# Performance work log

Measured on AMD Instinct MI355X. Metric: run time of the kernel, lower is better.

## Reference

```python
import jax, jax.numpy as jnp
import numpy as np

NEG = -1000000000.0

def setup_inputs() -> dict:
    key = jax.random.key(0)
    ks = jax.random.split(key, 6)
    B, V, F, H = 8, 4, 256, 768
    video_features = jax.random.normal(ks[0], (B, V, F, H), dtype=jnp.float32)
    video_attention_mask = jax.random.randint(ks[1], (B, V, F), 0, 2) > 0  # True = masked
    s = 1.0 / np.sqrt(H)
    Wqkv = jax.random.normal(ks[2], (3 * H, H), dtype=jnp.float32) * s
    bqkv = jax.random.normal(ks[3], (3 * H,), dtype=jnp.float32) * 0.01
    Wo = jax.random.normal(ks[4], (H, H), dtype=jnp.float32) * s
    bo = jax.random.normal(ks[5], (H,), dtype=jnp.float32) * 0.01
    return {"video_features": video_features, "video_attention_mask": video_attention_mask,
            "Wqkv": Wqkv, "bqkv": bqkv, "Wo": Wo, "bo": bo}

def reference(video_features, video_attention_mask, Wqkv, bqkv, Wo, bo):
    B, V, F, H = video_features.shape
    n_heads = 12
    head_dim = H // n_heads
    S = V * F  # total frames
    x = video_features.reshape(B, S, H)
    mask = video_attention_mask.reshape(B, S)
    # fused QKV projection (torch Linear: x @ W.T + b)
    qkv = x @ Wqkv.T + bqkv                      # [B, S, 3H]
    qkv = qkv.reshape(B, S, n_heads, 3 * head_dim).transpose(0, 2, 1, 3)  # [B, h, S, 3d]
    q, k, v = jnp.split(qkv, 3, axis=-1)         # each [B, h, S, d]
    scores = jnp.einsum('bhqd,bhkd->bhqk', q, k) / np.sqrt(head_dim)
    scores = jnp.where(mask[:, None, None, :], NEG, scores)
    attn = jax.nn.softmax(scores, axis=-1)       # dropout p=0 (eval) -> identity
    out = jnp.einsum('bhqk,bhkd->bhqd', attn, v) # [B, h, S, d]
    out = out.transpose(0, 2, 1, 3).reshape(B, S, H)
    out = out @ Wo.T + bo
    return out.reshape(B, V, F, H)
```

## Files before the change

### kernel.cpp

```cpp
#include <hip/hip_runtime.h>
#include <stdint.h>

typedef unsigned short u16;
typedef unsigned int u32;
typedef __attribute__((ext_vector_type(8))) unsigned short u16x8;
typedef __attribute__((ext_vector_type(4))) unsigned short u16x4;
typedef __attribute__((ext_vector_type(2))) unsigned int u32x2;
typedef __attribute__((ext_vector_type(4))) float f32x4;
typedef __attribute__((ext_vector_type(16))) float f32x16;
typedef __attribute__((ext_vector_type(4))) float floatx4;
typedef __attribute__((ext_vector_type(8))) __bf16 bf16x8;


__device__ __forceinline__ u16 f2bf(float f) {
  union { float f; unsigned u; } c; c.f = f;
  unsigned r = c.u + 0x7fffu + ((c.u >> 16) & 1u);
  return (u16)(r >> 16);
}

__device__ __forceinline__ u32 packbf2(float lo, float hi) {
  return (u32)f2bf(lo) | ((u32)f2bf(hi) << 16);
}

__device__ __forceinline__ u32 cvtpk(float lo, float hi) {
  u32 r;
  asm("v_cvt_pk_bf16_f32 %0, %1, %2" : "=v"(r) : "v"(lo), "v"(hi));
  return r;
}

__device__ __forceinline__ bf16x8 ld_bf8(const u16* p) {
  return __builtin_bit_cast(bf16x8, *(const u16x8*)p);
}

__device__ __forceinline__ float fexp2(float x) {
#if __has_builtin(__builtin_amdgcn_exp2f)
  return __builtin_amdgcn_exp2f(x);
#else
  float r; asm("v_exp_f32 %0, %1" : "=v"(r) : "v"(x)); return r;
#endif
}

__device__ __forceinline__ void glds16(const void* g, void* l) {
  __builtin_amdgcn_global_load_lds(
      (const __attribute__((address_space(1))) void*)g,
      (__attribute__((address_space(3))) void*)l, 16, 0, 0);
}

__global__ void convert_kernel(const float* __restrict__ x,
                               const float* __restrict__ w1,
                               const float* __restrict__ w2,
                               u16* __restrict__ xb,
                               u16* __restrict__ w1b,
                               u16* __restrict__ w2b) {
  const long NX = 6291456 / 4, NW1 = 1769472 / 4, NW2 = 589824 / 4;
  const long total = NX + NW1 + NW2;
  for (long i = (long)blockIdx.x * 256 + threadIdx.x; i < total;
       i += (long)gridDim.x * 256) {
    const float* src; u16* dst; long j;
    if (i < NX)            { src = x;  dst = xb;  j = i; }
    else if (i < NX + NW1) { src = w1; dst = w1b; j = i - NX; }
    else                   { src = w2; dst = w2b; j = i - NX - NW1; }
    floatx4 v = ((const floatx4*)src)[j];
    u16x4 o;
    o[0] = f2bf(v[0]); o[1] = f2bf(v[1]); o[2] = f2bf(v[2]); o[3] = f2bf(v[3]);
    ((u16x4*)dst)[j] = o;
  }
}

__global__ __launch_bounds__(256, 2)
void qkv_gemm(const u16* __restrict__ A, const u16* __restrict__ W,
              const float* __restrict__ bias,
              u16* __restrict__ qb, u16* __restrict__ kb, u16* __restrict__ vtb) {
  __shared__ __align__(16) u16 lds[30720];
  const int tid = threadIdx.x;
  const int lane = tid & 63, wid = tid >> 6;
  const int wm = wid >> 1, wn = wid & 1;
  const int l15 = lane & 15, l4 = lane >> 4;

  const int p = blockIdx.x;
  const int xcd = p & 7, i = p >> 3;
  const int by = xcd * 8 + i / 12;
  const int bx = i % 12;
  const int rowA0 = by * 128, rowB0 = bx * 192;

  const int rlo = lane >> 3;
  const u16* gA[2];
  const u16* gB[3];
#pragma unroll
  for (int c = 0; c < 2; ++c) {
    int mr = wid * 16 + c * 8 + rlo;
    int sl = (lane & 7) ^ (mr & 7);
    gA[c] = A + (size_t)(rowA0 + 2 * mr + (sl >> 2)) * 768 + (sl & 3) * 8;
  }
#pragma unroll
  for (int c = 0; c < 3; ++c) {
    int mr = wid * 24 + c * 8 + rlo;
    int sl = (lane & 7) ^ (mr & 7);
    gB[c] = W + (size_t)(rowB0 + 2 * mr + (sl >> 2)) * 768 + (sl & 3) * 8;
  }

  f32x4 acc[4][6];
  const f32x4 vz = {0.f, 0.f, 0.f, 0.f};
#pragma unroll
  for (int mi = 0; mi < 4; ++mi)
#pragma unroll
    for (int nj = 0; nj < 6; ++nj) acc[mi][nj] = vz;

#define QSTAGE(kb_, k0_)                                                   \
  {                                                                        \
    u16* bA_ = lds + (kb_) * 4096;                                         \
    u16* bB_ = lds + 12288 + (kb_) * 6144;                                 \
    _Pragma("unroll") for (int c = 0; c < 2; ++c)                          \
        glds16(gA[c] + (k0_), bA_ + (wid * 16 + c * 8) * 64);              \
    _Pragma("unroll") for (int c = 0; c < 3; ++c)                          \
        glds16(gB[c] + (k0_), bB_ + (wid * 24 + c * 8) * 64);              \
  }

  QSTAGE(0, 0);
  QSTAGE(1, 32);

  for (int ks = 0; ks < 24; ++ks) {
    const int cb = ks % 3;
    const u16* cA = lds + cb * 4096;
    const u16* cB = lds + 12288 + cb * 6144;

    __builtin_amdgcn_s_barrier();
    if (ks < 22) {
      QSTAGE((ks + 2) % 3, (ks + 2) * 32);
      asm volatile("s_waitcnt vmcnt(10)" ::: "memory");
    } else if (ks == 22) {
      asm volatile("s_waitcnt vmcnt(5)" ::: "memory");
    } else {
      asm volatile("s_waitcnt vmcnt(0)" ::: "memory");
    }
    __builtin_amdgcn_s_barrier();
    __builtin_amdgcn_sched_barrier(0);

    bf16x8 af[4], bfr[6];
#pragma unroll
    for (int mi = 0; mi < 4; ++mi) {
      int m = wm * 64 + mi * 16 + l15;
      int mr = m >> 1;
      int sp = ((m & 1) * 4 + l4) ^ (mr & 7);
      af[mi] = ld_bf8(cA + mr * 64 + sp * 8);
    }
#pragma unroll
    for (int nj = 0; nj < 6; ++nj) {
      int n = wn * 96 + nj * 16 + l15;
      int mr = n >> 1;
      int sp = ((n & 1) * 4 + l4) ^ (mr & 7);
      bfr[nj] = ld_bf8(cB + mr * 64 + sp * 8);
    }
    __builtin_amdgcn_s_setprio(1);
#pragma unroll
    for (int mi = 0; mi < 4; ++mi)
#pragma unroll
      for (int nj = 0; nj < 6; ++nj)
        acc[mi][nj] = __builtin_amdgcn_mfma_f32_16x16x32_bf16(
            af[mi], bfr[nj], acc[mi][nj], 0, 0, 0);
    __builtin_amdgcn_s_setprio(0);
  }
#undef QSTAGE

  const float QSC = 0.125f * 1.44269504088896f;
  const int batch = by >> 3, s0 = (by & 7) * 128;
  const size_t gbase = (size_t)(batch * 12 + bx) * 65536;

  float bias_v[6];
#pragma unroll
  for (int nj = 0; nj < 6; ++nj)
    bias_v[nj] = bias[rowB0 + wn * 96 + nj * 16 + l15];

  __syncthreads();

#pragma unroll
  for (int nj = 0; nj < 6; ++nj) {
    int col0 = wn * 96 + nj * 16;
    int band = col0 >> 6;
    int dd = (col0 & 63) + l15;
    float bv = bias_v[nj];
    if (band < 2) {
      float sc = (band == 0) ? QSC : 1.0f;
      u16* reg = lds + band * 9216;
#pragma unroll
      for (int mi = 0; mi < 4; ++mi)
#pragma unroll
        for (int r = 0; r < 4; ++r) {
          int m = wm * 64 + mi * 16 + l4 * 4 + r;
          reg[m * 72 + dd] = f2bf((acc[mi][nj][r] + bv) * sc);
        }
    } else {
      u16* reg = lds + 18432;
#pragma unroll
      for (int mi = 0; mi < 4; ++mi)
#pragma unroll
        for (int r = 0; r < 4; r += 2) {
          int m = wm * 64 + mi * 16 + l4 * 4 + r;
          *(u32*)&reg[dd * 136 + m] =
              packbf2(acc[mi][nj][r] + bv, acc[mi][nj][r + 1] + bv);
        }
    }
  }
  __syncthreads();

#pragma unroll
  for (int j = 0; j < 4; ++j) {
    int c = tid + j * 256;
    int m = c >> 3, dd0 = (c & 7) << 3;
    u16x8 v = *(const u16x8*)&lds[m * 72 + dd0];
    *(u16x8*)&qb[gbase + (size_t)(s0 + m) * 64 + dd0] = v;
  }
#pragma unroll
  for (int j = 0; j < 4; ++j) {
    int c = tid + j * 256;
    int m = c >> 3, dd0 = (c & 7) << 3;
    u16x8 v = *(const u16x8*)&lds[9216 + m * 72 + dd0];
    *(u16x8*)&kb[gbase + (size_t)(s0 + m) * 64 + dd0] = v;
  }
#pragma unroll
  for (int j = 0; j < 4; ++j) {
    int c = tid + j * 256;
    int dd = c >> 4, m0 = (c & 15) << 3;
    u16x8 v = *(const u16x8*)&lds[18432 + dd * 136 + m0];
    *(u16x8*)&vtb[gbase + (size_t)dd * 1024 + s0 + m0] = v;
  }
}

__global__ __launch_bounds__(256, 3)
void attn_kernel(const u16* __restrict__ qb, const u16* __restrict__ kb,
                 const u16* __restrict__ vtb, const void* __restrict__ maskp,
                 u16* __restrict__ x2) {
  const int bh = blockIdx.x, qt = blockIdx.y;
  const int b = bh / 12, h = bh - b * 12;
  const int tid = threadIdx.x;
  const int w = tid >> 6, lane = tid & 63;
  const int l31 = lane & 31, hi = lane >> 5;

  __shared__ float mbias[1024];
  __shared__ int any_big;
  __shared__ __align__(16) u16 plds[4][32][40];
  __shared__ __align__(16) u16 kvs[16384];

  if (tid == 0) any_big = 0;
  __syncthreads();
  {
    const unsigned* mu = (const unsigned*)maskp;
    int loc = 0;
    for (int i = tid; i < 2048; i += 256)
      if (mu[i] > 1u) loc = 1;
    if (loc) atomicOr(&any_big, 1);
  }
  __syncthreads();
  const float CEXP = 23.0831206542234f;
  if (any_big) {
    const unsigned char* mb = (const unsigned char*)maskp;
    for (int i = tid; i < 1024; i += 256)
      mbias[i] = mb[b * 1024 + i] ? -100000.0f : -CEXP;
  } else {
    const int* mi_ = (const int*)maskp;
    for (int i = tid; i < 1024; i += 256)
      mbias[i] = mi_[b * 1024 + i] ? -100000.0f : -CEXP;
  }

  const size_t base = (size_t)bh * 65536;
  const int q0w = qt * 128 + w * 32;

  const int rlo = lane >> 3;
  const int cg = (lane & 7) ^ (rlo & 7);
  const int srow = w * 8 + rlo;
  const u16* kg0 = kb + base + (size_t)srow * 64 + cg * 8;
  const u16* vg0 = vtb + base + (size_t)srow * 1024 + cg * 8;
  u16* kd0 = kvs + w * 512;
  u16* vd0 = kvs + 4096 + w * 512;

  bf16x8 qf[4];
#pragma unroll
  for (int dstep = 0; dstep < 4; ++dstep)
    qf[dstep] = ld_bf8(qb + base + (size_t)(q0w + l31) * 64 + dstep * 16 + hi * 8);

  f32x16 o[2];
#pragma unroll
  for (int dh = 0; dh < 2; ++dh)
#pragma unroll
    for (int r = 0; r < 16; ++r) o[dh][r] = 0.f;
  float ps = 0.f;

  glds16(kg0, kd0);
  glds16(kg0 + 32 * 64, kd0 + 2048);
  glds16(vg0, vd0);
  glds16(vg0 + 32 * 1024, vd0 + 2048);
  __syncthreads();

  for (int kt = 0; kt < 16; ++kt) {
    const int cur = kt & 1;
    if (kt < 15) {
      const int nxt = cur ^ 1;
      glds16(kg0 + (kt + 1) * 4096, kd0 + nxt * 8192);
      glds16(kg0 + (kt + 1) * 4096 + 32 * 64, kd0 + nxt * 8192 + 2048);
      glds16(vg0 + (kt + 1) * 64, vd0 + nxt * 8192);
      glds16(vg0 + (kt + 1) * 64 + 32 * 1024, vd0 + nxt * 8192 + 2048);
    }

    const u16* Kl = kvs + cur * 8192;
    const u16* Vl = kvs + cur * 8192 + 4096;

#pragma unroll
    for (int kk = 0; kk < 2; ++kk) {
      f32x16 s;
#pragma unroll
      for (int r = 0; r < 16; ++r) s[r] = 0.f;
      const int rk = kk * 32 + l31;
      __builtin_amdgcn_s_setprio(1);
#pragma unroll
      for (int dstep = 0; dstep < 4; ++dstep) {
        bf16x8 kf = ld_bf8(Kl + rk * 64 + ((dstep * 2 + hi) ^ (rk & 7)) * 8);
        s = __builtin_amdgcn_mfma_f32_32x32x16_bf16(kf, qf[dstep], s, 0, 0, 0);
      }
      __builtin_amdgcn_s_setprio(0);
#pragma unroll
      for (int g = 0; g < 4; ++g) {
        f32x4 bv = *(const f32x4*)(mbias + kt * 64 + kk * 32 + g * 8 + hi * 4);
        float p0 = fexp2(s[g * 4 + 0] + bv[0]);
        float p1 = fexp2(s[g * 4 + 1] + bv[1]);
        float p2 = fexp2(s[g * 4 + 2] + bv[2]);
        float p3 = fexp2(s[g * 4 + 3] + bv[3]);
        ps += (p0 + p1) + (p2 + p3);
        const int colb = g * 8 + hi * 4;
        *(u32*)&plds[w][l31][colb]     = cvtpk(p0, p1);
        *(u32*)&plds[w][l31][colb + 2] = cvtpk(p2, p3);
      }

      __builtin_amdgcn_s_setprio(1);
#pragma unroll
      for (int t = 0; t < 2; ++t) {
        bf16x8 pf = ld_bf8(&plds[w][l31][t * 16 + hi * 8]);
#pragma unroll
        for (int dh = 0; dh < 2; ++dh) {
          const int rv = dh * 32 + l31;
          const int gv = kk * 4 + t * 2 + hi;
          bf16x8 vf = ld_bf8(Vl + rv * 64 + (gv ^ (rv & 7)) * 8);
          o[dh] = __builtin_amdgcn_mfma_f32_32x32x16_bf16(vf, pf, o[dh], 0, 0, 0);
        }
      }
      __builtin_amdgcn_s_setprio(0);
    }

    __syncthreads();
  }

  ps += __shfl_xor(ps, 32, 64);
  float inv = 1.0f / ps;

  u16* obuf = kvs + w * 2304;
#pragma unroll
  for (int dh = 0; dh < 2; ++dh)
#pragma unroll
    for (int j = 0; j < 8; ++j) {
      u32 v = cvtpk(o[dh][2 * j] * inv, o[dh][2 * j + 1] * inv);
      int col = dh * 32 + 8 * (j >> 1) + 4 * hi + 2 * (j & 1);
      *(u32*)(obuf + l31 * 72 + col) = v;
    }

  {
    int row2 = lane >> 1, ch = lane & 1;
    const u16* srcp = obuf + row2 * 72 + ch * 32;
    u16x8 t0 = *(const u16x8*)(srcp);
    u16x8 t1 = *(const u16x8*)(srcp + 8);
    u16x8 t2 = *(const u16x8*)(srcp + 16);
    u16x8 t3 = *(const u16x8*)(srcp + 24);
    size_t m = (size_t)b * 1024 + qt * 128 + w * 32 + row2;
    u16* dst = x2 + m * 768 + h * 64 + ch * 32;
    *(u16x8*)dst = t0;
    *(u16x8*)(dst + 8) = t1;
    *(u16x8*)(dst + 16) = t2;
    *(u16x8*)(dst + 24) = t3;
  }
}

__global__ __launch_bounds__(256, 2)
void out_gemm(const u16* __restrict__ A, const u16* __restrict__ W,
              const float* __restrict__ bias, float* __restrict__ out) {
  __shared__ __align__(16) u16 lds[24576];
  const int tid = threadIdx.x;
  const int lane = tid & 63, wid = tid >> 6;
  const int wm = wid >> 1, wn = wid & 1;
  const int l15 = lane & 15, l4 = lane >> 4;

  const int p = blockIdx.x;
  const int xcd = p & 7, i = p >> 3;
  const int by = xcd * 16 + (i >> 2);
  const int bx = i & 3;
  const int rowA0 = by * 64, rowB0 = bx * 192;

  const int rlo = lane >> 3;
  const u16* gA0;
  {
    int mr = wid * 8 + rlo;
    int sl = (lane & 7) ^ (mr & 7);
    gA0 = A + (size_t)(rowA0 + 2 * mr + (sl >> 2)) * 768 + (sl & 3) * 8;
  }
  const u16* gB[3];
#pragma unroll
  for (int c = 0; c < 3; ++c) {
    int mr = wid * 24 + c * 8 + rlo;
    int sl = (lane & 7) ^ (mr & 7);
    gB[c] = W + (size_t)(rowB0 + 2 * mr + (sl >> 2)) * 768 + (sl & 3) * 8;
  }

  f32x4 acc[2][6];
  const f32x4 vz = {0.f, 0.f, 0.f, 0.f};
#pragma unroll
  for (int mi = 0; mi < 2; ++mi)
#pragma unroll
    for (int nj = 0; nj < 6; ++nj) acc[mi][nj] = vz;

#define OSTAGE(kb_, k0_)                                                   \
  {                                                                        \
    u16* bA_ = lds + (kb_) * 2048;                                         \
    u16* bB_ = lds + 6144 + (kb_) * 6144;                                  \
    glds16(gA0 + (k0_), bA_ + (wid * 8) * 64);                             \
    _Pragma("unroll") for (int c = 0; c < 3; ++c)                          \
        glds16(gB[c] + (k0_), bB_ + (wid * 24 + c * 8) * 64);              \
  }

  OSTAGE(0, 0);
  OSTAGE(1, 32);

  for (int ks = 0; ks < 24; ++ks) {
    const int cb = ks % 3;
    const u16* cA = lds + cb * 2048;
    const u16* cB = lds + 6144 + cb * 6144;

    __builtin_amdgcn_s_barrier();
    if (ks < 22) {
      OSTAGE((ks + 2) % 3, (ks + 2) * 32);
      asm volatile("s_waitcnt vmcnt(8)" ::: "memory");
    } else if (ks == 22) {
      asm volatile("s_waitcnt vmcnt(4)" ::: "memory");
    } else {
      asm volatile("s_waitcnt vmcnt(0)" ::: "memory");
    }
    __builtin_amdgcn_s_barrier();
    __builtin_amdgcn_sched_barrier(0);

    bf16x8 af[2], bfr[6];
#pragma unroll
    for (int mi = 0; mi < 2; ++mi) {
      int m = wm * 32 + mi * 16 + l15;
      int mr = m >> 1;
      int sp = ((m & 1) * 4 + l4) ^ (mr & 7);
      af[mi] = ld_bf8(cA + mr * 64 + sp * 8);
    }
#pragma unroll
    for (int nj = 0; nj < 6; ++nj) {
      int n = wn * 96 + nj * 16 + l15;
      int mr = n >> 1;
      int sp = ((n & 1) * 4 + l4) ^ (mr & 7);
      bfr[nj] = ld_bf8(cB + mr * 64 + sp * 8);
    }
    __builtin_amdgcn_s_setprio(1);
#pragma unroll
    for (int mi = 0; mi < 2; ++mi)
#pragma unroll
      for (int nj = 0; nj < 6; ++nj)
        acc[mi][nj] = __builtin_amdgcn_mfma_f32_16x16x32_bf16(
            af[mi], bfr[nj], acc[mi][nj], 0, 0, 0);
    __builtin_amdgcn_s_setprio(0);
  }
#undef OSTAGE

#pragma unroll
  for (int nj = 0; nj < 6; ++nj) {
    int n = rowB0 + wn * 96 + nj * 16 + l15;
    float bn_ = bias[n];
#pragma unroll
    for (int mi = 0; mi < 2; ++mi)
#pragma unroll
      for (int r = 0; r < 4; ++r) {
        int m = rowA0 + wm * 32 + mi * 16 + l4 * 4 + r;
        out[(size_t)m * 768 + n] = acc[mi][nj][r] + bn_;
      }
  }
}

extern "C" void kernel_launch(void* const* d_in, const int* in_sizes, int n_in,
                              void* d_out, int out_size, void* d_ws, size_t ws_size,
                              hipStream_t stream) {
  const float* x    = (const float*)d_in[0];
  const void*  mask = d_in[1];
  const float* wqkv = (const float*)d_in[2];
  const float* bqkv = (const float*)d_in[3];
  const float* wo   = (const float*)d_in[4];
  const float* bo   = (const float*)d_in[5];
  float* out = (float*)d_out;

  u16* ws = (u16*)d_ws;
  u16* xbf   = ws;
  u16* wqkvb = ws + 6291456;
  u16* wob   = ws + 8060928;
  u16* qbuf  = ws + 8650752;
  u16* kbuf  = ws + 14942208;
  u16* vtbuf = ws + 21233664;
  u16* x2buf = ws + 27525120;

  convert_kernel<<<2048, 256, 0, stream>>>(x, wqkv, wo, xbf, wqkvb, wob);
  qkv_gemm<<<768, 256, 0, stream>>>(xbf, wqkvb, bqkv, qbuf, kbuf, vtbuf);
  attn_kernel<<<dim3(96, 8), 256, 0, stream>>>(qbuf, kbuf, vtbuf, mask, x2buf);
  out_gemm<<<512, 256, 0, stream>>>(x2buf, wob, bo, out);
}
```

Before: 115.5 us.

## Process two 32-row query tiles per wave to reuse K/V fragments

Each attention wave now owns 64 query rows instead of 32. It loads the K and V fragments from LDS once and applies them to two sets of Q fragments and accumulators. The grid's query-tile dimension halves and launch bounds drop to 2 blocks per CU to make room for the extra registers. This cuts LDS reads and per-tile overhead per unit of work, at the cost of fewer blocks (384) and lower occupancy, which may leave CUs idle or expose latency.

After: 118.1 us. +2.3%, slower.

```diff
diff --git a/kernel.cpp b/kernel.cpp
--- a/kernel.cpp
+++ b/kernel.cpp
@@ -226,7 +226,7 @@
   }
 }
 
-__global__ __launch_bounds__(256, 3)
+__global__ __launch_bounds__(256, 2)
 void attn_kernel(const u16* __restrict__ qb, const u16* __restrict__ kb,
                  const u16* __restrict__ vtb, const void* __restrict__ maskp,
                  u16* __restrict__ x2) {
@@ -263,7 +263,7 @@
   }
 
   const size_t base = (size_t)bh * 65536;
-  const int q0w = qt * 128 + w * 32;
+  const int q0w = qt * 256 + w * 64;
 
   const int rlo = lane >> 3;
   const int cg = (lane & 7) ^ (rlo & 7);
@@ -273,23 +273,48 @@
   u16* kd0 = kvs + w * 512;
   u16* vd0 = kvs + 4096 + w * 512;
 
-  bf16x8 qf[4];
-#pragma unroll
-  for (int dstep = 0; dstep < 4; ++dstep)
-    qf[dstep] = ld_bf8(qb + base + (size_t)(q0w + l31) * 64 + dstep * 16 + hi * 8);
-
-  f32x16 o[2];
+  bf16x8 qf0[4], qf1[4];
+#pragma unroll
+  for (int ds = 0; ds < 4; ++ds) {
+    qf0[ds] = ld_bf8(qb + base + (size_t)(q0w + l31) * 64 + ds * 16 + hi * 8);
+    qf1[ds] = ld_bf8(qb + base + (size_t)(q0w + 32 + l31) * 64 + ds * 16 + hi * 8);
+  }
+
+  f32x16 o0[2], o1[2];
 #pragma unroll
   for (int dh = 0; dh < 2; ++dh)
 #pragma unroll
-    for (int r = 0; r < 16; ++r) o[dh][r] = 0.f;
-  float ps = 0.f;
+    for (int r = 0; r < 16; ++r) { o0[dh][r] = 0.f; o1[dh][r] = 0.f; }
+  float ps0 = 0.f, ps1 = 0.f;
 
   glds16(kg0, kd0);
   glds16(kg0 + 32 * 64, kd0 + 2048);
   glds16(vg0, vd0);
   glds16(vg0 + 32 * 1024, vd0 + 2048);
   __syncthreads();
+
+#define SMPV(SV, OD, PS)                                                     \
+  {                                                                          \
+    _Pragma("unroll") for (int g = 0; g < 4; ++g) {                          \
+      f32x4 bv = *(const f32x4*)(mbias + kt * 64 + kk * 32 + g * 8 + hi * 4);\
+      float p0 = fexp2(SV[g * 4 + 0] + bv[0]);                               \
+      float p1 = fexp2(SV[g * 4 + 1] + bv[1]);                               \
+      float p2 = fexp2(SV[g * 4 + 2] + bv[2]);                               \
+      float p3 = fexp2(SV[g * 4 + 3] + bv[3]);                               \
+      PS += (p0 + p1) + (p2 + p3);                                           \
+      const int colb = g * 8 + hi * 4;                                       \
+      *(u32*)&plds[w][l31][colb]     = cvtpk(p0, p1);                        \
+      *(u32*)&plds[w][l31][colb + 2] = cvtpk(p2, p3);                        \
+    }                                                                        \
+    __builtin_amdgcn_s_setprio(1);                                           \
+    _Pragma("unroll") for (int t = 0; t < 2; ++t) {                          \
+      bf16x8 pf = ld_bf8(&plds[w][l31][t * 16 + hi * 8]);                    \
+      _Pragma("unroll") for (int dh = 0; dh < 2; ++dh)                       \
+        OD[dh] = __builtin_amdgcn_mfma_f32_32x32x16_bf16(vf[t][dh], pf,      \
+                                                         OD[dh], 0, 0, 0);   \
+    }                                                                        \
+    __builtin_amdgcn_s_setprio(0);                                           \
+  }
 
   for (int kt = 0; kt < 16; ++kt) {
     const int cur = kt & 1;
@@ -306,74 +331,73 @@
 
 #pragma unroll
     for (int kk = 0; kk < 2; ++kk) {
-      f32x16 s;
-#pragma unroll
-      for (int r = 0; r < 16; ++r) s[r] = 0.f;
       const int rk = kk * 32 + l31;
+      bf16x8 kf[4];
+#pragma unroll
+      for (int ds = 0; ds < 4; ++ds)
+        kf[ds] = ld_bf8(Kl + rk * 64 + ((ds * 2 + hi) ^ (rk & 7)) * 8);
+
+      f32x16 s0, s1;
+#pragma unroll
+      for (int r = 0; r < 16; ++r) { s0[r] = 0.f; s1[r] = 0.f; }
       __builtin_amdgcn_s_setprio(1);
 #pragma unroll
-      for (int dstep = 0; dstep < 4; ++dstep) {
-        bf16x8 kf = ld_bf8(Kl + rk * 64 + ((dstep * 2 + hi) ^ (rk & 7)) * 8);
-        s = __builtin_amdgcn_mfma_f32_32x32x16_bf16(kf, qf[dstep], s, 0, 0, 0);
-      }
+      for (int ds = 0; ds < 4; ++ds)
+        s0 = __builtin_amdgcn_mfma_f32_32x32x16_bf16(kf[ds], qf0[ds], s0, 0, 0, 0);
+#pragma unroll
+      for (int ds = 0; ds < 4; ++ds)
+        s1 = __builtin_amdgcn_mfma_f32_32x32x16_bf16(kf[ds], qf1[ds], s1, 0, 0, 0);
       __builtin_amdgcn_s_setprio(0);
-#pragma unroll
-      for (int g = 0; g < 4; ++g) {
-        f32x4 bv = *(const f32x4*)(mbias + kt * 64 + kk * 32 + g * 8 + hi * 4);
-        float p0 = fexp2(s[g * 4 + 0] + bv[0]);
-        float p1 = fexp2(s[g * 4 + 1] + bv[1]);
-        float p2 = fexp2(s[g * 4 + 2] + bv[2]);
-        float p3 = fexp2(s[g * 4 + 3] + bv[3]);
-        ps += (p0 + p1) + (p2 + p3);
-        const int colb = g * 8 + hi * 4;
-        *(u32*)&plds[w][l31][colb]     = cvtpk(p0, p1);
-        *(u32*)&plds[w][l31][colb + 2] = cvtpk(p2, p3);
-      }
-
-      __builtin_amdgcn_s_setprio(1);
-#pragma unroll
-      for (int t = 0; t < 2; ++t) {
-        bf16x8 pf = ld_bf8(&plds[w][l31][t * 16 + hi * 8]);
+
+      bf16x8 vf[2][2];
+#pragma unroll
+      for (int t = 0; t < 2; ++t)
 #pragma unroll
         for (int dh = 0; dh < 2; ++dh) {
           const int rv = dh * 32 + l31;
           const int gv = kk * 4 + t * 2 + hi;
-          bf16x8 vf = ld_bf8(Vl + rv * 64 + (gv ^ (rv & 7)) * 8);
-          o[dh] = __builtin_amdgcn_mfma_f32_32x32x16_bf16(vf, pf, o[dh], 0, 0, 0);
+          vf[t][dh] = ld_bf8(Vl + rv * 64 + (gv ^ (rv & 7)) * 8);
         }
+
+      SMPV(s0, o0, ps0);
+      SMPV(s1, o1, ps1);
+    }
+
+    __syncthreads();
+  }
+#undef SMPV
+
+  ps0 += __shfl_xor(ps0, 32, 64);
+  ps1 += __shfl_xor(ps1, 32, 64);
+  float inv0 = 1.0f / ps0, inv1 = 1.0f / ps1;
+
+  u16* obuf = kvs + w * 2304;
+#pragma unroll
+  for (int half = 0; half < 2; ++half) {
+    const f32x16* oh = half ? o1 : o0;
+    float inv = half ? inv1 : inv0;
+#pragma unroll
+    for (int dh = 0; dh < 2; ++dh)
+#pragma unroll
+      for (int j = 0; j < 8; ++j) {
+        u32 v = cvtpk(oh[dh][2 * j] * inv, oh[dh][2 * j + 1] * inv);
+        int col = dh * 32 + 8 * (j >> 1) + 4 * hi + 2 * (j & 1);
+        *(u32*)(obuf + l31 * 72 + col) = v;
       }
-      __builtin_amdgcn_s_setprio(0);
-    }
-
-    __syncthreads();
-  }
-
-  ps += __shfl_xor(ps, 32, 64);
-  float inv = 1.0f / ps;
-
-  u16* obuf = kvs + w * 2304;
-#pragma unroll
-  for (int dh = 0; dh < 2; ++dh)
-#pragma unroll
-    for (int j = 0; j < 8; ++j) {
-      u32 v = cvtpk(o[dh][2 * j] * inv, o[dh][2 * j + 1] * inv);
-      int col = dh * 32 + 8 * (j >> 1) + 4 * hi + 2 * (j & 1);
-      *(u32*)(obuf + l31 * 72 + col) = v;
-    }
-
-  {
-    int row2 = lane >> 1, ch = lane & 1;
-    const u16* srcp = obuf + row2 * 72 + ch * 32;
-    u16x8 t0 = *(const u16x8*)(srcp);
-    u16x8 t1 = *(const u16x8*)(srcp + 8);
-    u16x8 t2 = *(const u16x8*)(srcp + 16);
-    u16x8 t3 = *(const u16x8*)(srcp + 24);
-    size_t m = (size_t)b * 1024 + qt * 128 + w * 32 + row2;
-    u16* dst = x2 + m * 768 + h * 64 + ch * 32;
-    *(u16x8*)dst = t0;
-    *(u16x8*)(dst + 8) = t1;
-    *(u16x8*)(dst + 16) = t2;
-    *(u16x8*)(dst + 24) = t3;
+    {
+      int row2 = lane >> 1, ch = lane & 1;
+      const u16* srcp = obuf + row2 * 72 + ch * 32;
+      u16x8 t0 = *(const u16x8*)(srcp);
+      u16x8 t1 = *(const u16x8*)(srcp + 8);
+      u16x8 t2 = *(const u16x8*)(srcp + 16);
+      u16x8 t3 = *(const u16x8*)(srcp + 24);
+      size_t m = (size_t)b * 1024 + q0w + half * 32 + row2;
+      u16* dst = x2 + m * 768 + h * 64 + ch * 32;
+      *(u16x8*)dst = t0;
+      *(u16x8*)(dst + 8) = t1;
+      *(u16x8*)(dst + 16) = t2;
+      *(u16x8*)(dst + 24) = t3;
+    }
   }
 }
 
@@ -505,6 +529,6 @@
 
   convert_kernel<<<2048, 256, 0, stream>>>(x, wqkv, wo, xbf, wqkvb, wob);
   qkv_gemm<<<768, 256, 0, stream>>>(xbf, wqkvb, bqkv, qbuf, kbuf, vtbuf);
-  attn_kernel<<<dim3(96, 8), 256, 0, stream>>>(qbuf, kbuf, vtbuf, mask, x2buf);
+  attn_kernel<<<dim3(96, 4), 256, 0, stream>>>(qbuf, kbuf, vtbuf, mask, x2buf);
   out_gemm<<<512, 256, 0, stream>>>(x2buf, wob, bo, out);
 }
```
